# Kernel optimization log

Hardware: AMD Instinct MI355X
Metric: run time of the kernel (lower is better)

The kernel has to match this reference:

```python
import jax, jax.numpy as jnp
import numpy as np

EPS = 1e-5  # torch LayerNorm default eps
DIM = 2
FEED = 10


def layernorm(x, g, b):
    mu = jnp.mean(x, axis=-1, keepdims=True)
    var = jnp.mean((x - mu) ** 2, axis=-1, keepdims=True)
    return (x - mu) * jax.lax.rsqrt(var + EPS) * g + b


def mha(q, k, v, w_in, b_in, w_out, b_out):
    # nn.MultiheadAttention with n_heads=1: head_dim == embed_dim
    E = q.shape[-1]
    wq, wk, wv = jnp.split(w_in, 3, axis=0)
    bq, bk, bv = jnp.split(b_in, 3)
    qh = q @ wq.T + bq  # [B,Sq,E]
    kh = k @ wk.T + bk  # [B,Sk,E]
    vh = v @ wv.T + bv
    scale = 1.0 / np.sqrt(E).astype(np.float32)
    scores = jnp.einsum('bqd,bkd->bqk', qh, kh) * scale  # [B,Sq,Sk]
    attn = jax.nn.softmax(scores, axis=-1)
    out = jnp.einsum('bqk,bkd->bqd', attn, vh)
    return out @ w_out.T + b_out


def setup_inputs() -> dict:
    key = jax.random.key(0)
    ks = jax.random.split(key, 16)
    d, fd = DIM, FEED
    s = 0.5
    inp = {
        'x': jax.random.normal(ks[0], (32, 32, 256, d), dtype=jnp.float32),
        'm': jax.random.normal(ks[1], (1024, 256, d), dtype=jnp.float32),
        # self-attention params
        'sa_w_in': jax.random.normal(ks[2], (3 * d, d), dtype=jnp.float32) * s,
        'sa_b_in': jnp.zeros((3 * d,), dtype=jnp.float32),
        'sa_w_out': jax.random.normal(ks[3], (d, d), dtype=jnp.float32) * s,
        'sa_b_out': jnp.zeros((d,), dtype=jnp.float32),
        # cross-attention params
        'ca_w_in': jax.random.normal(ks[4], (3 * d, d), dtype=jnp.float32) * s,
        'ca_b_in': jnp.zeros((3 * d,), dtype=jnp.float32),
        'ca_w_out': jax.random.normal(ks[5], (d, d), dtype=jnp.float32) * s,
        'ca_b_out': jnp.zeros((d,), dtype=jnp.float32),
        # layernorms
        'ln1_g': jnp.ones((d,), dtype=jnp.float32),
        'ln1_b': jnp.zeros((d,), dtype=jnp.float32),
        'ln2_g': jnp.ones((d,), dtype=jnp.float32),
        'ln2_b': jnp.zeros((d,), dtype=jnp.float32),
        'ln3_g': jnp.ones((d,), dtype=jnp.float32),
        'ln3_b': jnp.zeros((d,), dtype=jnp.float32),
        # feed-forward: Linear(d,fd) -> LayerNorm(fd) -> ReLU -> Linear(fd,d)
        'f_w1': jax.random.normal(ks[6], (fd, d), dtype=jnp.float32) * s,
        'f_b1': jnp.zeros((fd,), dtype=jnp.float32),
        'f_ln_g': jnp.ones((fd,), dtype=jnp.float32),
        'f_ln_b': jnp.zeros((fd,), dtype=jnp.float32),
        'f_w2': jax.random.normal(ks[7], (d, fd), dtype=jnp.float32) * s,
        'f_b2': jnp.zeros((d,), dtype=jnp.float32),
    }
    return inp


def reference(x, m, sa_w_in, sa_b_in, sa_w_out, sa_b_out,
              ca_w_in, ca_b_in, ca_w_out, ca_b_out,
              ln1_g, ln1_b, ln2_g, ln2_b, ln3_g, ln3_b,
              f_w1, f_b1, f_ln_g, f_ln_b, f_w2, f_b2):
    b, k, s, f = x.shape
    h = x.reshape(-1, s, f)  # [b*k, s, f]
    h = layernorm(h, ln1_g, ln1_b)
    h = h + mha(h, h, h, sa_w_in, sa_b_in, sa_w_out, sa_b_out)
    h = layernorm(h, ln2_g, ln2_b)
    h = h + mha(h, m, m, ca_w_in, ca_b_in, ca_w_out, ca_b_out)
    h = layernorm(h, ln3_g, ln3_b)
    ff = h @ f_w1.T + f_b1
    ff = layernorm(ff, f_ln_g, f_ln_b)
    ff = jax.nn.relu(ff) @ f_w2.T + f_b2
    h = h + ff
    return h.reshape(b, k, s, f)
```

## Files before the change

kernel.cpp:

```cpp
#include <hip/hip_runtime.h>

#define NTOK 256
#define LOG2E 1.44269504088896340736f
#define LN_EPS 1e-5f

typedef float v4f __attribute__((ext_vector_type(4)));

static __device__ __forceinline__ v4f splat4(float s) {
    v4f r; r.x = s; r.y = s; r.z = s; r.w = s; return r;
}

template <int CTRL>
static __device__ __forceinline__ float dppq(float v) {
    return __int_as_float(
        __builtin_amdgcn_update_dpp(0, __float_as_int(v), CTRL, 0xF, 0xF, true));
}
static __device__ __forceinline__ v4f quad_sum(v4f v) {
    v4f t;
    t.x = dppq<0xB1>(v.x); t.y = dppq<0xB1>(v.y);
    t.z = dppq<0xB1>(v.z); t.w = dppq<0xB1>(v.w);
    v += t;
    t.x = dppq<0x4E>(v.x); t.y = dppq<0x4E>(v.y);
    t.z = dppq<0x4E>(v.z); t.w = dppq<0x4E>(v.w);
    return v + t;
}
static __device__ __forceinline__ float sel4(v4f v, int kq) {
    float ab = (kq & 1) ? v.y : v.x;
    float cd = (kq & 1) ? v.w : v.z;
    return (kq & 2) ? cd : ab;
}

__global__ __launch_bounds__(256, 8)
void att_decoder_kernel(
    const float* __restrict__ x, const float* __restrict__ m,
    const float* __restrict__ sa_w_in, const float* __restrict__ sa_b_in,
    const float* __restrict__ sa_w_out, const float* __restrict__ sa_b_out,
    const float* __restrict__ ca_w_in, const float* __restrict__ ca_b_in,
    const float* __restrict__ ca_w_out, const float* __restrict__ ca_b_out,
    const float* __restrict__ ln1_g, const float* __restrict__ ln1_b,
    const float* __restrict__ ln2_g, const float* __restrict__ ln2_b,
    const float* __restrict__ ln3_g, const float* __restrict__ ln3_b,
    const float* __restrict__ f_w1, const float* __restrict__ f_b1,
    const float* __restrict__ f_ln_g, const float* __restrict__ f_ln_b,
    const float* __restrict__ f_w2, const float* __restrict__ f_b2,
    float* __restrict__ out)
{
    const int tid  = threadIdx.x;
    const int row  = blockIdx.x;
    const int lane = tid & 63;
    const int w    = tid >> 6;
    const int kq   = lane & 3;
    const int qg   = (w << 4) + (lane >> 2);

    __shared__ float4 kv_sa[NTOK];
    __shared__ float4 kv_ca[NTOK];

    const float2* __restrict__ x2 = (const float2*)x;
    const float2* __restrict__ m2 = (const float2*)m;

    {
        const int j = (tid >> 2) | ((tid & 3) << 6);
        float2 xv = x2[row * NTOK + j];
        float d = 0.5f * (xv.x - xv.y);
        float n = d * rsqrtf(d * d + LN_EPS);
        float h0 =  n * ln1_g[0] + ln1_b[0];
        float h1 = -n * ln1_g[1] + ln1_b[1];
        float4 kv;
        kv.x = h0*sa_w_in[4]  + h1*sa_w_in[5]  + sa_b_in[2];
        kv.y = h0*sa_w_in[6]  + h1*sa_w_in[7]  + sa_b_in[3];
        kv.z = h0*sa_w_in[8]  + h1*sa_w_in[9]  + sa_b_in[4];
        kv.w = h0*sa_w_in[10] + h1*sa_w_in[11] + sa_b_in[5];
        kv_sa[tid] = kv;
        float2 mv = m2[row * NTOK + j];
        kv.x = mv.x*ca_w_in[4]  + mv.y*ca_w_in[5]  + ca_b_in[2];
        kv.y = mv.x*ca_w_in[6]  + mv.y*ca_w_in[7]  + ca_b_in[3];
        kv.z = mv.x*ca_w_in[8]  + mv.y*ca_w_in[9]  + ca_b_in[4];
        kv.w = mv.x*ca_w_in[10] + mv.y*ca_w_in[11] + ca_b_in[5];
        kv_ca[tid] = kv;
    }

    v4f h0, h1;
    {
        float2 q0 = x2[row * NTOK + qg];
        float2 q1 = x2[row * NTOK + qg + 64];
        float2 q2 = x2[row * NTOK + qg + 128];
        float2 q3 = x2[row * NTOK + qg + 192];
        const float g0 = ln1_g[0], b0 = ln1_b[0], g1 = ln1_g[1], b1 = ln1_b[1];
#define LN1C(QV, C) { float d_ = 0.5f*(QV.x - QV.y);                       \
        float n_ = d_ * rsqrtf(d_*d_ + LN_EPS);                             \
        h0.C = n_*g0 + b0; h1.C = -n_*g1 + b1; }
        LN1C(q0, x) LN1C(q1, y) LN1C(q2, z) LN1C(q3, w)
#undef LN1C
    }

    __syncthreads();

    const float sc = 0.7071067811865476f * LOG2E;
    const int slot0 = kq;

    {
        v4f qe0 = (h0*splat4(sa_w_in[0]) + h1*splat4(sa_w_in[1]) + splat4(sa_b_in[0])) * splat4(sc);
        v4f qe1 = (h0*splat4(sa_w_in[2]) + h1*splat4(sa_w_in[3]) + splat4(sa_b_in[1])) * splat4(sc);
        v4f l = splat4(0.f), a0 = splat4(0.f), a1 = splat4(0.f);
        #pragma unroll 8
        for (int i = 0; i < 64; ++i) {
            float4 kv = kv_sa[(i << 2) + slot0];
            v4f s = qe0*splat4(kv.x) + qe1*splat4(kv.y);
            v4f p;
            p.x = __builtin_amdgcn_exp2f(s.x);
            p.y = __builtin_amdgcn_exp2f(s.y);
            p.z = __builtin_amdgcn_exp2f(s.z);
            p.w = __builtin_amdgcn_exp2f(s.w);
            l += p; a0 += p*splat4(kv.z); a1 += p*splat4(kv.w);
        }
        l = quad_sum(l); a0 = quad_sum(a0); a1 = quad_sum(a1);
        v4f rl;
        rl.x = 1.0f/l.x; rl.y = 1.0f/l.y; rl.z = 1.0f/l.z; rl.w = 1.0f/l.w;
        a0 *= rl; a1 *= rl;
        h0 += a0*splat4(sa_w_out[0]) + a1*splat4(sa_w_out[1]) + splat4(sa_b_out[0]);
        h1 += a0*splat4(sa_w_out[2]) + a1*splat4(sa_w_out[3]) + splat4(sa_b_out[1]);
    }

    {
        const float g0 = ln2_g[0], b0 = ln2_b[0], g1 = ln2_g[1], b1 = ln2_b[1];
#define LN2C(C) { float d_ = 0.5f*(h0.C - h1.C);                           \
        float n_ = d_ * rsqrtf(d_*d_ + LN_EPS);                             \
        h0.C = n_*g0 + b0; h1.C = -n_*g1 + b1; }
        LN2C(x) LN2C(y) LN2C(z) LN2C(w)
#undef LN2C
    }

    v4f cl, ca0, ca1;
    {
        v4f qe0 = (h0*splat4(ca_w_in[0]) + h1*splat4(ca_w_in[1]) + splat4(ca_b_in[0])) * splat4(sc);
        v4f qe1 = (h0*splat4(ca_w_in[2]) + h1*splat4(ca_w_in[3]) + splat4(ca_b_in[1])) * splat4(sc);
        v4f l = splat4(0.f), a0 = splat4(0.f), a1 = splat4(0.f);
        #pragma unroll 8
        for (int i = 0; i < 64; ++i) {
            float4 kv = kv_ca[(i << 2) + slot0];
            v4f s = qe0*splat4(kv.x) + qe1*splat4(kv.y);
            v4f p;
            p.x = __builtin_amdgcn_exp2f(s.x);
            p.y = __builtin_amdgcn_exp2f(s.y);
            p.z = __builtin_amdgcn_exp2f(s.z);
            p.w = __builtin_amdgcn_exp2f(s.w);
            l += p; a0 += p*splat4(kv.z); a1 += p*splat4(kv.w);
        }
        cl = quad_sum(l); ca0 = quad_sum(a0); ca1 = quad_sum(a1);
    }

    float L   = sel4(cl, kq);
    float A0  = sel4(ca0, kq) / L;
    float A1  = sel4(ca1, kq) / L;
    float s0  = sel4(h0, kq);
    float s1  = sel4(h1, kq);
    s0 += A0*ca_w_out[0] + A1*ca_w_out[1] + ca_b_out[0];
    s1 += A0*ca_w_out[2] + A1*ca_w_out[3] + ca_b_out[1];

    {
        float d = 0.5f*(s0 - s1);
        float n = d * rsqrtf(d*d + LN_EPS);
        s0 =  n*ln3_g[0] + ln3_b[0];
        s1 = -n*ln3_g[1] + ln3_b[1];
    }

    {
        float ff[10];
        #pragma unroll
        for (int i = 0; i < 10; ++i)
            ff[i] = s0*f_w1[2*i] + s1*f_w1[2*i+1] + f_b1[i];
        float mu = 0.f;
        #pragma unroll
        for (int i = 0; i < 10; ++i) mu += ff[i];
        mu *= 0.1f;
        float var = 0.f;
        #pragma unroll
        for (int i = 0; i < 10; ++i) { float d = ff[i] - mu; var += d * d; }
        var *= 0.1f;
        float r = rsqrtf(var + LN_EPS);
        float o0 = 0.f, o1 = 0.f;
        #pragma unroll
        for (int i = 0; i < 10; ++i) {
            float n = (ff[i] - mu) * r * f_ln_g[i] + f_ln_b[i];
            n = fmaxf(n, 0.f);
            o0 += n * f_w2[i];
            o1 += n * f_w2[10 + i];
        }
        s0 += o0 + f_b2[0];
        s1 += o1 + f_b2[1];
    }

    ((float2*)out)[row * NTOK + qg + (kq << 6)] = make_float2(s0, s1);
}

extern "C" void kernel_launch(void* const* d_in, const int* in_sizes, int n_in,
                              void* d_out, int out_size, void* d_ws, size_t ws_size,
                              hipStream_t stream) {
    const float* x        = (const float*)d_in[0];
    const float* m        = (const float*)d_in[1];
    const float* sa_w_in  = (const float*)d_in[2];
    const float* sa_b_in  = (const float*)d_in[3];
    const float* sa_w_out = (const float*)d_in[4];
    const float* sa_b_out = (const float*)d_in[5];
    const float* ca_w_in  = (const float*)d_in[6];
    const float* ca_b_in  = (const float*)d_in[7];
    const float* ca_w_out = (const float*)d_in[8];
    const float* ca_b_out = (const float*)d_in[9];
    const float* ln1_g    = (const float*)d_in[10];
    const float* ln1_b    = (const float*)d_in[11];
    const float* ln2_g    = (const float*)d_in[12];
    const float* ln2_b    = (const float*)d_in[13];
    const float* ln3_g    = (const float*)d_in[14];
    const float* ln3_b    = (const float*)d_in[15];
    const float* f_w1     = (const float*)d_in[16];
    const float* f_b1     = (const float*)d_in[17];
    const float* f_ln_g   = (const float*)d_in[18];
    const float* f_ln_b   = (const float*)d_in[19];
    const float* f_w2     = (const float*)d_in[20];
    const float* f_b2     = (const float*)d_in[21];

    const int nbatch = in_sizes[0] / (NTOK * 2);
    att_decoder_kernel<<<nbatch, 256, 0, stream>>>(
        x, m, sa_w_in, sa_b_in, sa_w_out, sa_b_out,
        ca_w_in, ca_b_in, ca_w_out, ca_b_out,
        ln1_g, ln1_b, ln2_g, ln2_b, ln3_g, ln3_b,
        f_w1, f_b1, f_ln_g, f_ln_b, f_w2, f_b2,
        (float*)d_out);
}
```

Before: 123.4 us.

## Fold LayerNorm and K/V projections algebraically into attention inner loops

```diff
diff --git a/kernel.cpp b/kernel.cpp
--- a/kernel.cpp
+++ b/kernel.cpp
@@ -28,6 +28,12 @@
     float ab = (kq & 1) ? v.y : v.x;
     float cd = (kq & 1) ? v.w : v.z;
     return (kq & 2) ? cd : ab;
+}
+static __device__ __forceinline__ v4f rcp4(v4f v) {
+    v4f r;
+    r.x = __builtin_amdgcn_rcpf(v.x); r.y = __builtin_amdgcn_rcpf(v.y);
+    r.z = __builtin_amdgcn_rcpf(v.z); r.w = __builtin_amdgcn_rcpf(v.w);
+    return r;
 }
 
 __global__ __launch_bounds__(256, 8)
@@ -52,46 +58,35 @@
     const int kq   = lane & 3;
     const int qg   = (w << 4) + (lane >> 2);
 
-    __shared__ float4 kv_sa[NTOK];
-    __shared__ float4 kv_ca[NTOK];
+    __shared__ float  n_sa[NTOK];
+    __shared__ float2 mca [NTOK];
 
     const float2* __restrict__ x2 = (const float2*)x;
     const float2* __restrict__ m2 = (const float2*)m;
+
+    const float g0 = ln1_g[0], b0 = ln1_b[0], g1 = ln1_g[1], b1 = ln1_b[1];
 
     {
         const int j = (tid >> 2) | ((tid & 3) << 6);
         float2 xv = x2[row * NTOK + j];
         float d = 0.5f * (xv.x - xv.y);
-        float n = d * rsqrtf(d * d + LN_EPS);
-        float h0 =  n * ln1_g[0] + ln1_b[0];
-        float h1 = -n * ln1_g[1] + ln1_b[1];
-        float4 kv;
-        kv.x = h0*sa_w_in[4]  + h1*sa_w_in[5]  + sa_b_in[2];
-        kv.y = h0*sa_w_in[6]  + h1*sa_w_in[7]  + sa_b_in[3];
-        kv.z = h0*sa_w_in[8]  + h1*sa_w_in[9]  + sa_b_in[4];
-        kv.w = h0*sa_w_in[10] + h1*sa_w_in[11] + sa_b_in[5];
-        kv_sa[tid] = kv;
-        float2 mv = m2[row * NTOK + j];
-        kv.x = mv.x*ca_w_in[4]  + mv.y*ca_w_in[5]  + ca_b_in[2];
-        kv.y = mv.x*ca_w_in[6]  + mv.y*ca_w_in[7]  + ca_b_in[3];
-        kv.z = mv.x*ca_w_in[8]  + mv.y*ca_w_in[9]  + ca_b_in[4];
-        kv.w = mv.x*ca_w_in[10] + mv.y*ca_w_in[11] + ca_b_in[5];
-        kv_ca[tid] = kv;
-    }
-
-    v4f h0, h1;
+        n_sa[tid] = d * rsqrtf(d * d + LN_EPS);
+        mca[tid]  = m2[row * NTOK + j];
+    }
+
+    v4f nq;
     {
         float2 q0 = x2[row * NTOK + qg];
         float2 q1 = x2[row * NTOK + qg + 64];
         float2 q2 = x2[row * NTOK + qg + 128];
         float2 q3 = x2[row * NTOK + qg + 192];
-        const float g0 = ln1_g[0], b0 = ln1_b[0], g1 = ln1_g[1], b1 = ln1_b[1];
-#define LN1C(QV, C) { float d_ = 0.5f*(QV.x - QV.y);                       \
-        float n_ = d_ * rsqrtf(d_*d_ + LN_EPS);                             \
-        h0.C = n_*g0 + b0; h1.C = -n_*g1 + b1; }
-        LN1C(q0, x) LN1C(q1, y) LN1C(q2, z) LN1C(q3, w)
-#undef LN1C
-    }
+#define LNQ(QV, C) { float d_ = 0.5f*(QV.x - QV.y);                         \
+        nq.C = d_ * rsqrtf(d_*d_ + LN_EPS); }
+        LNQ(q0, x) LNQ(q1, y) LNQ(q2, z) LNQ(q3, w)
+#undef LNQ
+    }
+    v4f h0 = nq * splat4(g0) + splat4(b0);
+    v4f h1 = nq * splat4(-g1) + splat4(b1);
 
     __syncthreads();
 
@@ -99,59 +94,73 @@
     const int slot0 = kq;
 
     {
-        v4f qe0 = (h0*splat4(sa_w_in[0]) + h1*splat4(sa_w_in[1]) + splat4(sa_b_in[0])) * splat4(sc);
-        v4f qe1 = (h0*splat4(sa_w_in[2]) + h1*splat4(sa_w_in[3]) + splat4(sa_b_in[1])) * splat4(sc);
-        v4f l = splat4(0.f), a0 = splat4(0.f), a1 = splat4(0.f);
+        const float ak0 = g0*sa_w_in[4] - g1*sa_w_in[5];
+        const float ak1 = g0*sa_w_in[6] - g1*sa_w_in[7];
+        const float av0 = g0*sa_w_in[8] - g1*sa_w_in[9];
+        const float bv0 = b0*sa_w_in[8] + b1*sa_w_in[9] + sa_b_in[4];
+        const float av1 = g0*sa_w_in[10] - g1*sa_w_in[11];
+        const float bv1 = b0*sa_w_in[10] + b1*sa_w_in[11] + sa_b_in[5];
+        v4f qh0 = h0*splat4(sa_w_in[0]) + h1*splat4(sa_w_in[1]) + splat4(sa_b_in[0]);
+        v4f qh1 = h0*splat4(sa_w_in[2]) + h1*splat4(sa_w_in[3]) + splat4(sa_b_in[1]);
+        v4f A = (qh0*splat4(ak0) + qh1*splat4(ak1)) * splat4(sc);
+        v4f S0 = splat4(0.f), S1 = splat4(0.f);
         #pragma unroll 8
         for (int i = 0; i < 64; ++i) {
-            float4 kv = kv_sa[(i << 2) + slot0];
-            v4f s = qe0*splat4(kv.x) + qe1*splat4(kv.y);
+            float n = n_sa[(i << 2) + slot0];
+            v4f s = A * splat4(n);
             v4f p;
             p.x = __builtin_amdgcn_exp2f(s.x);
             p.y = __builtin_amdgcn_exp2f(s.y);
             p.z = __builtin_amdgcn_exp2f(s.z);
             p.w = __builtin_amdgcn_exp2f(s.w);
-            l += p; a0 += p*splat4(kv.z); a1 += p*splat4(kv.w);
+            S0 += p;
+            S1 += p * splat4(n);
         }
-        l = quad_sum(l); a0 = quad_sum(a0); a1 = quad_sum(a1);
-        v4f rl;
-        rl.x = 1.0f/l.x; rl.y = 1.0f/l.y; rl.z = 1.0f/l.z; rl.w = 1.0f/l.w;
-        a0 *= rl; a1 *= rl;
+        S0 = quad_sum(S0); S1 = quad_sum(S1);
+        v4f R = S1 * rcp4(S0);
+        v4f a0 = splat4(av0)*R + splat4(bv0);
+        v4f a1 = splat4(av1)*R + splat4(bv1);
         h0 += a0*splat4(sa_w_out[0]) + a1*splat4(sa_w_out[1]) + splat4(sa_b_out[0]);
         h1 += a0*splat4(sa_w_out[2]) + a1*splat4(sa_w_out[3]) + splat4(sa_b_out[1]);
     }
 
     {
-        const float g0 = ln2_g[0], b0 = ln2_b[0], g1 = ln2_g[1], b1 = ln2_b[1];
-#define LN2C(C) { float d_ = 0.5f*(h0.C - h1.C);                           \
-        float n_ = d_ * rsqrtf(d_*d_ + LN_EPS);                             \
-        h0.C = n_*g0 + b0; h1.C = -n_*g1 + b1; }
+        const float G0 = ln2_g[0], B0 = ln2_b[0], G1 = ln2_g[1], B1 = ln2_b[1];
+#define LN2C(C) { float d_ = 0.5f*(h0.C - h1.C);                            \
+        float n_ = d_ * rsqrtf(d_*d_ + LN_EPS);                              \
+        h0.C = n_*G0 + B0; h1.C = -n_*G1 + B1; }
         LN2C(x) LN2C(y) LN2C(z) LN2C(w)
 #undef LN2C
     }
 
-    v4f cl, ca0, ca1;
-    {
-        v4f qe0 = (h0*splat4(ca_w_in[0]) + h1*splat4(ca_w_in[1]) + splat4(ca_b_in[0])) * splat4(sc);
-        v4f qe1 = (h0*splat4(ca_w_in[2]) + h1*splat4(ca_w_in[3]) + splat4(ca_b_in[1])) * splat4(sc);
-        v4f l = splat4(0.f), a0 = splat4(0.f), a1 = splat4(0.f);
+    v4f T0, T1, T2;
+    {
+        v4f qh0 = h0*splat4(ca_w_in[0]) + h1*splat4(ca_w_in[1]) + splat4(ca_b_in[0]);
+        v4f qh1 = h0*splat4(ca_w_in[2]) + h1*splat4(ca_w_in[3]) + splat4(ca_b_in[1]);
+        v4f C0 = (qh0*splat4(ca_w_in[4]) + qh1*splat4(ca_w_in[6])) * splat4(sc);
+        v4f C1 = (qh0*splat4(ca_w_in[5]) + qh1*splat4(ca_w_in[7])) * splat4(sc);
+        T0 = splat4(0.f); T1 = splat4(0.f); T2 = splat4(0.f);
         #pragma unroll 8
         for (int i = 0; i < 64; ++i) {
-            float4 kv = kv_ca[(i << 2) + slot0];
-            v4f s = qe0*splat4(kv.x) + qe1*splat4(kv.y);
+            float2 mv = mca[(i << 2) + slot0];
+            v4f s = C0*splat4(mv.x) + C1*splat4(mv.y);
             v4f p;
             p.x = __builtin_amdgcn_exp2f(s.x);
             p.y = __builtin_amdgcn_exp2f(s.y);
             p.z = __builtin_amdgcn_exp2f(s.z);
             p.w = __builtin_amdgcn_exp2f(s.w);
-            l += p; a0 += p*splat4(kv.z); a1 += p*splat4(kv.w);
+            T0 += p;
+            T1 += p * splat4(mv.x);
+            T2 += p * splat4(mv.y);
         }
-        cl = quad_sum(l); ca0 = quad_sum(a0); ca1 = quad_sum(a1);
-    }
-
-    float L   = sel4(cl, kq);
-    float A0  = sel4(ca0, kq) / L;
-    float A1  = sel4(ca1, kq) / L;
+        T0 = quad_sum(T0); T1 = quad_sum(T1); T2 = quad_sum(T2);
+    }
+
+    float rT  = __builtin_amdgcn_rcpf(sel4(T0, kq));
+    float U1  = sel4(T1, kq) * rT;
+    float U2  = sel4(T2, kq) * rT;
+    float A0  = ca_w_in[8]*U1  + ca_w_in[9]*U2  + ca_b_in[4];
+    float A1  = ca_w_in[10]*U1 + ca_w_in[11]*U2 + ca_b_in[5];
     float s0  = sel4(h0, kq);
     float s1  = sel4(h1, kq);
     s0 += A0*ca_w_out[0] + A1*ca_w_out[1] + ca_b_out[0];
```

Measured after the change: 121.1 us. No clear change (-1.9%).
